# Kernel tuning notes

Hardware: AMD Instinct MI355X
Metric: run time of the kernel (lower is better)

Reference implementation:

```python
import jax, jax.numpy as jnp
import numpy as np

B, L, C = 4, 2048, 1024
A_SCALE = 0.1  # keep cumulative 2x2 matrix products bounded over L steps


def setup_inputs() -> dict:
    key = jax.random.key(0)
    kA, kX = jax.random.split(key)
    # last dim of size 2 = (real, imag), matching complex_to_real layout
    A = jax.random.normal(kA, (B, L, C, 2, 2, 2), dtype=jnp.float32) * A_SCALE
    X = jax.random.normal(kX, (B, L, C, 2, 2, 2), dtype=jnp.float32)
    return {"A": A, "X": X}


def _to_complex(r):
    return jax.lax.complex(r[..., 0], r[..., 1])


def _to_real(z):
    return jnp.stack([jnp.real(z), jnp.imag(z)], axis=-1)


def reference(A, X):
    # A, X: [B, L, C, 2, 2, 2] real pairs -> [B, L, C, 2, 2] complex64
    Ac = _to_complex(A)
    Xc = _to_complex(X)

    # Inclusive scan of the linear recurrence Y_t = A_t @ Y_{t-1} + X_t, Y_0 = X_0.
    # combine(earlier, later): (A_l @ A_e, A_l @ X_e + X_l) -- matches the Triton
    # mat2x2_scan_combine where c = B@A and z = B@X + Y.
    def combine(e, l):
        Ae, Xe = e
        Al, Xl = l
        A_out = jnp.einsum('blcij,blcjk->blcik', Al, Ae)
        X_out = jnp.einsum('blcij,blcjk->blcik', Al, Xe) + Xl
        return (A_out, X_out)

    _, Yc = jax.lax.associative_scan(combine, (Ac, Xc), axis=1)
    return _to_real(Yc)  # [B, L, C, 2, 2, 2]
```

## Files before the change

### kernel.cpp

```cpp
#include <hip/hip_runtime.h>

#define BB   4
#define LL   2048
#define CC   1024
#define NSEG 64
#define SEGLEN (LL / NSEG)
#define CBLK 256
#define CG   (CC / CBLK)

struct Cplx { float r, i; };

__device__ __forceinline__ Cplx cmul(Cplx a, Cplx b) {
    Cplx o;
    o.r = fmaf(a.r, b.r, -a.i * b.i);
    o.i = fmaf(a.r, b.i,  a.i * b.r);
    return o;
}
__device__ __forceinline__ Cplx cfma(Cplx a, Cplx b, Cplx acc) {
    acc.r = fmaf(a.r, b.r, fmaf(-a.i, b.i, acc.r));
    acc.i = fmaf(a.r, b.i, fmaf( a.i, b.r, acc.i));
    return acc;
}

__device__ __forceinline__ void load_mat(const float* __restrict__ p, Cplx m[4]) {
    const float4* p4 = (const float4*)p;
    float4 v0 = p4[0];
    float4 v1 = p4[1];
    m[0].r = v0.x; m[0].i = v0.y;
    m[1].r = v0.z; m[1].i = v0.w;
    m[2].r = v1.x; m[2].i = v1.y;
    m[3].r = v1.z; m[3].i = v1.w;
}
__device__ __forceinline__ void store_mat(float* __restrict__ p, const Cplx m[4]) {
    float4* p4 = (float4*)p;
    p4[0] = make_float4(m[0].r, m[0].i, m[1].r, m[1].i);
    p4[1] = make_float4(m[2].r, m[2].i, m[3].r, m[3].i);
}

__device__ __forceinline__ void matmul(const Cplx a[4], const Cplx m[4], Cplx out[4]) {
    #pragma unroll
    for (int ik = 0; ik < 4; ++ik) {
        int i = ik >> 1, k = ik & 1;
        Cplx t = cmul(a[i * 2 + 0], m[0 * 2 + k]);
        out[ik] = cfma(a[i * 2 + 1], m[1 * 2 + k], t);
    }
}
__device__ __forceinline__ void matmul_add(const Cplx a[4], const Cplx m[4],
                                           const Cplx x[4], Cplx out[4]) {
    #pragma unroll
    for (int ik = 0; ik < 4; ++ik) {
        int i = ik >> 1, k = ik & 1;
        Cplx t = cfma(a[i * 2 + 0], m[0 * 2 + k], x[ik]);
        out[ik] = cfma(a[i * 2 + 1], m[1 * 2 + k], t);
    }
}

__global__ __launch_bounds__(256) void pscan_pass1(const float* __restrict__ A,
                                                   const float* __restrict__ X,
                                                   float* __restrict__ ws) {
    int bid = blockIdx.x;
    int cg = bid % CG;
    int s  = (bid / CG) % NSEG;
    int b  = bid / (CG * NSEG);
    int c  = cg * CBLK + threadIdx.x;

    long l0   = (long)s * SEGLEN;
    long base = (((long)b * LL + l0) * CC + c) * 8;
    const long step = (long)CC * 8;

    Cplx Ac[4], Xc[4];
    load_mat(A + base, Ac);
    load_mat(X + base, Xc);
    base += step;

    #pragma unroll 4
    for (int t = 1; t < SEGLEN; ++t, base += step) {
        Cplx a[4], x[4], nA[4], nX[4];
        load_mat(A + base, a);
        load_mat(X + base, x);
        matmul(a, Ac, nA);
        matmul_add(a, Xc, x, nX);
        #pragma unroll
        for (int j = 0; j < 4; ++j) { Ac[j] = nA[j]; Xc[j] = nX[j]; }
    }

    float* w = ws + (((long)b * NSEG + s) * CC + c) * 16;
    store_mat(w,     Ac);
    store_mat(w + 8, Xc);
}

__global__ __launch_bounds__(256) void pscan_pass2(float* __restrict__ ws) {
    int t = blockIdx.x * blockDim.x + threadIdx.x;
    int b = t / CC;
    int c = t % CC;

    Cplx Y[4];
    #pragma unroll
    for (int j = 0; j < 4; ++j) { Y[j].r = 0.f; Y[j].i = 0.f; }

    for (int s = 0; s < NSEG; ++s) {
        float* w = ws + (((long)b * NSEG + s) * CC + c) * 16;
        Cplx Ac[4], Xc[4];
        load_mat(w,     Ac);
        load_mat(w + 8, Xc);
        store_mat(w, Y);
        Cplx nY[4];
        matmul_add(Ac, Y, Xc, nY);
        #pragma unroll
        for (int j = 0; j < 4; ++j) Y[j] = nY[j];
    }
}

__global__ __launch_bounds__(256) void pscan_pass3(const float* __restrict__ A,
                                                   const float* __restrict__ X,
                                                   const float* __restrict__ ws,
                                                   float* __restrict__ out) {
    int bid = blockIdx.x;
    int cg = bid % CG;
    int s  = (bid / CG) % NSEG;
    int b  = bid / (CG * NSEG);
    int c  = cg * CBLK + threadIdx.x;

    const float* w = ws + (((long)b * NSEG + s) * CC + c) * 16;
    Cplx Y[4];
    load_mat(w, Y);

    long l0   = (long)s * SEGLEN;
    long base = (((long)b * LL + l0) * CC + c) * 8;
    const long step = (long)CC * 8;

    #pragma unroll 4
    for (int t = 0; t < SEGLEN; ++t, base += step) {
        Cplx a[4], x[4], nY[4];
        load_mat(A + base, a);
        load_mat(X + base, x);
        matmul_add(a, Y, x, nY);
        #pragma unroll
        for (int j = 0; j < 4; ++j) Y[j] = nY[j];
        store_mat(out + base, Y);
    }
}

extern "C" void kernel_launch(void* const* d_in, const int* in_sizes, int n_in,
                              void* d_out, int out_size, void* d_ws, size_t ws_size,
                              hipStream_t stream) {
    const float* A = (const float*)d_in[0];
    const float* X = (const float*)d_in[1];
    float* out = (float*)d_out;
    float* ws  = (float*)d_ws;

    dim3 blk(256);
    pscan_pass1<<<BB * NSEG * CG, blk, 0, stream>>>(A, X, ws);
    pscan_pass2<<<(BB * CC) / 256, blk, 0, stream>>>(ws);
    pscan_pass3<<<BB * NSEG * CG, blk, 0, stream>>>(A, X, ws, out);
}
```

Baseline: 739.6 us.

## Replace three-pass scan with single-pass decoupled look-back kernel

Merges the three-pass segmented scan (reduce, serial carry propagation, rescan) into one kernel. Blocks take work through an atomic ticket and publish per-segment aggregates or inclusive prefixes under flags, and later blocks walk back to pick up their carry. This drops the serial pass2 and two launch boundaries, so the second read of A and X is more likely to hit cache. Segments shrink to 16 steps to give more parallelism, and nontemporal loads and stores are used in the output phase. The cost is spin-wait latency, more flag and workspace traffic, and reliance on the ticket ordering to avoid deadlock.

```diff
diff --git a/kernel.cpp b/kernel.cpp
--- a/kernel.cpp
+++ b/kernel.cpp
@@ -3,10 +3,15 @@
 #define BB   4
 #define LL   2048
 #define CC   1024
-#define NSEG 64
-#define SEGLEN (LL / NSEG)
-#define CBLK 256
-#define CG   (CC / CBLK)
+#define CHB  256
+#define CG   (CC / CHB)
+#define NROWS (BB * CG)
+#define SEGLEN 16
+#define NSEG (LL / SEGLEN)
+#define NBLK (NROWS * NSEG)
+
+
+typedef float v4f __attribute__((ext_vector_type(4)));
 
 struct Cplx { float r, i; };
 
@@ -23,18 +28,29 @@
 }
 
 __device__ __forceinline__ void load_mat(const float* __restrict__ p, Cplx m[4]) {
-    const float4* p4 = (const float4*)p;
-    float4 v0 = p4[0];
-    float4 v1 = p4[1];
-    m[0].r = v0.x; m[0].i = v0.y;
-    m[1].r = v0.z; m[1].i = v0.w;
-    m[2].r = v1.x; m[2].i = v1.y;
-    m[3].r = v1.z; m[3].i = v1.w;
+    const v4f* p4 = (const v4f*)p;
+    v4f v0 = p4[0], v1 = p4[1];
+    m[0].r = v0.x; m[0].i = v0.y; m[1].r = v0.z; m[1].i = v0.w;
+    m[2].r = v1.x; m[2].i = v1.y; m[3].r = v1.z; m[3].i = v1.w;
+}
+__device__ __forceinline__ void load_mat_nt(const float* __restrict__ p, Cplx m[4]) {
+    const v4f* p4 = (const v4f*)p;
+    v4f v0 = __builtin_nontemporal_load(p4);
+    v4f v1 = __builtin_nontemporal_load(p4 + 1);
+    m[0].r = v0.x; m[0].i = v0.y; m[1].r = v0.z; m[1].i = v0.w;
+    m[2].r = v1.x; m[2].i = v1.y; m[3].r = v1.z; m[3].i = v1.w;
 }
 __device__ __forceinline__ void store_mat(float* __restrict__ p, const Cplx m[4]) {
-    float4* p4 = (float4*)p;
-    p4[0] = make_float4(m[0].r, m[0].i, m[1].r, m[1].i);
-    p4[1] = make_float4(m[2].r, m[2].i, m[3].r, m[3].i);
+    v4f* p4 = (v4f*)p;
+    p4[0] = (v4f){m[0].r, m[0].i, m[1].r, m[1].i};
+    p4[1] = (v4f){m[2].r, m[2].i, m[3].r, m[3].i};
+}
+__device__ __forceinline__ void store_mat_nt(float* __restrict__ p, const Cplx m[4]) {
+    v4f* p4 = (v4f*)p;
+    v4f v0 = {m[0].r, m[0].i, m[1].r, m[1].i};
+    v4f v1 = {m[2].r, m[2].i, m[3].r, m[3].i};
+    __builtin_nontemporal_store(v0, p4);
+    __builtin_nontemporal_store(v1, p4 + 1);
 }
 
 __device__ __forceinline__ void matmul(const Cplx a[4], const Cplx m[4], Cplx out[4]) {
@@ -55,89 +71,133 @@
     }
 }
 
-__global__ __launch_bounds__(256) void pscan_pass1(const float* __restrict__ A,
-                                                   const float* __restrict__ X,
-                                                   float* __restrict__ ws) {
-    int bid = blockIdx.x;
-    int cg = bid % CG;
-    int s  = (bid / CG) % NSEG;
-    int b  = bid / (CG * NSEG);
-    int c  = cg * CBLK + threadIdx.x;
-
-    long l0   = (long)s * SEGLEN;
-    long base = (((long)b * LL + l0) * CC + c) * 8;
+__global__ void pscan_init(int* __restrict__ w) {
+    int i = blockIdx.x * blockDim.x + threadIdx.x;
+    if (i < 4096) w[i] = 0;
+}
+
+__global__ __launch_bounds__(256) void pscan_lookback(const float* __restrict__ A,
+                                                      const float* __restrict__ X,
+                                                      float* __restrict__ out,
+                                                      float* __restrict__ ws) {
+    __shared__ int sh_wid;
+    __shared__ int sh_f;
+    int*   ticket = (int*)ws;
+    int*   flags  = (int*)ws + 16;
+    float* agg    = ws + 4096;
+    float* incl   = ws + 4096 + (long)NBLK * CHB * 16;
+
+    if (threadIdx.x == 0) sh_wid = atomicAdd(ticket, 1);
+    __syncthreads();
+    const int wid = sh_wid;
+    const int seg = wid / NROWS;
+    const int row = wid % NROWS;
+    const int b   = row / CG;
+    const int cg  = row % CG;
+    const int c   = cg * CHB + threadIdx.x;
+
     const long step = (long)CC * 8;
+    long base = (((long)b * LL + (long)seg * SEGLEN) * CC + c) * 8;
 
     Cplx Ac[4], Xc[4];
     load_mat(A + base, Ac);
     load_mat(X + base, Xc);
-    base += step;
-
-    #pragma unroll 4
-    for (int t = 1; t < SEGLEN; ++t, base += step) {
-        Cplx a[4], x[4], nA[4], nX[4];
-        load_mat(A + base, a);
-        load_mat(X + base, x);
-        matmul(a, Ac, nA);
-        matmul_add(a, Xc, x, nX);
+    {
+        long p = base + step;
+        #pragma unroll 4
+        for (int t = 1; t < SEGLEN; ++t, p += step) {
+            Cplx a[4], x[4], nA[4], nX[4];
+            load_mat(A + p, a);
+            load_mat(X + p, x);
+            matmul(a, Ac, nA);
+            matmul_add(a, Xc, x, nX);
+            #pragma unroll
+            for (int j = 0; j < 4; ++j) { Ac[j] = nA[j]; Xc[j] = nX[j]; }
+        }
+    }
+
+    const long slot   = ((long)row * NSEG + seg) * CHB + threadIdx.x;
+    const int  myFlag = row * NSEG + seg;
+
+    Cplx carry[4];
+
+    if (seg == 0) {
         #pragma unroll
-        for (int j = 0; j < 4; ++j) { Ac[j] = nA[j]; Xc[j] = nX[j]; }
-    }
-
-    float* w = ws + (((long)b * NSEG + s) * CC + c) * 16;
-    store_mat(w,     Ac);
-    store_mat(w + 8, Xc);
-}
-
-__global__ __launch_bounds__(256) void pscan_pass2(float* __restrict__ ws) {
-    int t = blockIdx.x * blockDim.x + threadIdx.x;
-    int b = t / CC;
-    int c = t % CC;
+        for (int j = 0; j < 4; ++j) { carry[j].r = 0.f; carry[j].i = 0.f; }
+        store_mat(incl + slot * 8, Xc);
+        __threadfence();
+        __syncthreads();
+        if (threadIdx.x == 0)
+            __hip_atomic_store(&flags[myFlag], 2, __ATOMIC_RELEASE, __HIP_MEMORY_SCOPE_AGENT);
+    } else {
+        float* ag = agg + slot * 16;
+        store_mat(ag,     Ac);
+        store_mat(ag + 8, Xc);
+        __threadfence();
+        __syncthreads();
+        if (threadIdx.x == 0)
+            __hip_atomic_store(&flags[myFlag], 1, __ATOMIC_RELEASE, __HIP_MEMORY_SCOPE_AGENT);
+
+        Cplx AT[4], XT[4];
+        AT[0] = {1.f, 0.f}; AT[1] = {0.f, 0.f};
+        AT[2] = {0.f, 0.f}; AT[3] = {1.f, 0.f};
+        #pragma unroll
+        for (int j = 0; j < 4; ++j) { XT[j].r = 0.f; XT[j].i = 0.f; }
+
+        int p = seg - 1;
+        for (;;) {
+            if (threadIdx.x == 0) {
+                int f;
+                while ((f = __hip_atomic_load(&flags[row * NSEG + p],
+                                              __ATOMIC_ACQUIRE,
+                                              __HIP_MEMORY_SCOPE_AGENT)) < 1)
+                    __builtin_amdgcn_s_sleep(1);
+                sh_f = f;
+            }
+            __syncthreads();
+            const int f = sh_f;
+            const long ps = ((long)row * NSEG + p) * CHB + threadIdx.x;
+            if (f == 2) {
+                Cplx Yp[4];
+                load_mat(incl + ps * 8, Yp);
+                matmul_add(AT, Yp, XT, carry);
+                break;
+            } else {
+                Cplx Ap[4], Xp[4], nA[4], nX[4];
+                const float* ag2 = agg + ps * 16;
+                load_mat(ag2,     Ap);
+                load_mat(ag2 + 8, Xp);
+                matmul(AT, Ap, nA);
+                matmul_add(AT, Xp, XT, nX);
+                #pragma unroll
+                for (int j = 0; j < 4; ++j) { AT[j] = nA[j]; XT[j] = nX[j]; }
+                --p;
+            }
+            __syncthreads();
+        }
+
+        Cplx Yi[4];
+        matmul_add(Ac, carry, Xc, Yi);
+        store_mat(incl + slot * 8, Yi);
+        __threadfence();
+        __syncthreads();
+        if (threadIdx.x == 0)
+            __hip_atomic_store(&flags[myFlag], 2, __ATOMIC_RELEASE, __HIP_MEMORY_SCOPE_AGENT);
+    }
 
     Cplx Y[4];
     #pragma unroll
-    for (int j = 0; j < 4; ++j) { Y[j].r = 0.f; Y[j].i = 0.f; }
-
-    for (int s = 0; s < NSEG; ++s) {
-        float* w = ws + (((long)b * NSEG + s) * CC + c) * 16;
-        Cplx Ac[4], Xc[4];
-        load_mat(w,     Ac);
-        load_mat(w + 8, Xc);
-        store_mat(w, Y);
-        Cplx nY[4];
-        matmul_add(Ac, Y, Xc, nY);
-        #pragma unroll
-        for (int j = 0; j < 4; ++j) Y[j] = nY[j];
-    }
-}
-
-__global__ __launch_bounds__(256) void pscan_pass3(const float* __restrict__ A,
-                                                   const float* __restrict__ X,
-                                                   const float* __restrict__ ws,
-                                                   float* __restrict__ out) {
-    int bid = blockIdx.x;
-    int cg = bid % CG;
-    int s  = (bid / CG) % NSEG;
-    int b  = bid / (CG * NSEG);
-    int c  = cg * CBLK + threadIdx.x;
-
-    const float* w = ws + (((long)b * NSEG + s) * CC + c) * 16;
-    Cplx Y[4];
-    load_mat(w, Y);
-
-    long l0   = (long)s * SEGLEN;
-    long base = (((long)b * LL + l0) * CC + c) * 8;
-    const long step = (long)CC * 8;
-
-    #pragma unroll 4
+    for (int j = 0; j < 4; ++j) Y[j] = carry[j];
+
+    #pragma unroll 2
     for (int t = 0; t < SEGLEN; ++t, base += step) {
         Cplx a[4], x[4], nY[4];
-        load_mat(A + base, a);
-        load_mat(X + base, x);
+        load_mat_nt(A + base, a);
+        load_mat_nt(X + base, x);
         matmul_add(a, Y, x, nY);
         #pragma unroll
         for (int j = 0; j < 4; ++j) Y[j] = nY[j];
-        store_mat(out + base, Y);
+        store_mat_nt(out + base, Y);
     }
 }
 
@@ -149,8 +209,6 @@
     float* out = (float*)d_out;
     float* ws  = (float*)d_ws;
 
-    dim3 blk(256);
-    pscan_pass1<<<BB * NSEG * CG, blk, 0, stream>>>(A, X, ws);
-    pscan_pass2<<<(BB * CC) / 256, blk, 0, stream>>>(ws);
-    pscan_pass3<<<BB * NSEG * CG, blk, 0, stream>>>(A, X, ws, out);
-}
+    pscan_init<<<16, 256, 0, stream>>>((int*)ws);
+    pscan_lookback<<<NBLK, 256, 0, stream>>>(A, X, out, ws);
+}
```

After: 2.302 ms. +211.3%, slower.
